# Kernel optimization log

Measured on AMD Instinct MI355X. Metric: run time of the kernel, lower is better.

Reference implementation:

```python
import jax, jax.numpy as jnp
import numpy as np

IN, H, OUT, T, B = 132, 1024, 132, 100, 256


def setup_inputs() -> dict:
    key = jax.random.key(0)
    ks = jax.random.split(key, 16)
    s_in = 1.0 / np.sqrt(H)
    def mk(k, shape):
        return jax.random.uniform(k, shape, jnp.float32, -s_in, s_in)
    inp = {
        "real_seq": jax.random.normal(ks[0], (B, T, IN), jnp.float32),
        "W_ih1": mk(ks[1], (4 * H, IN)), "W_hh1": mk(ks[2], (4 * H, H)),
        "b_ih1": mk(ks[3], (4 * H,)),   "b_hh1": mk(ks[4], (4 * H,)),
        "W_ih2": mk(ks[5], (4 * H, H)), "W_hh2": mk(ks[6], (4 * H, H)),
        "b_ih2": mk(ks[7], (4 * H,)),   "b_hh2": mk(ks[8], (4 * H,)),
        "W_ih3": mk(ks[9], (4 * H, H)), "W_hh3": mk(ks[10], (4 * H, H)),
        "b_ih3": mk(ks[11], (4 * H,)),  "b_hh3": mk(ks[12], (4 * H,)),
        "W_dec": mk(ks[13], (OUT, H)),  "b_dec": mk(ks[14], (OUT,)),
        "condition_num": 5, "groundtruth_num": 5,
    }
    return inp


def _lstm_cell(x, h, c, W_ih, W_hh, b_ih, b_hh):
    # torch LSTMCell: gates in (i, f, g, o) order
    gates = x @ W_ih.T + b_ih + h @ W_hh.T + b_hh
    i, f, g, o = jnp.split(gates, 4, axis=-1)
    i, f, o = jax.nn.sigmoid(i), jax.nn.sigmoid(f), jax.nn.sigmoid(o)
    g = jnp.tanh(g)
    c_new = f * c + i * g
    h_new = o * jnp.tanh(c_new)
    return h_new, c_new


def reference(real_seq, W_ih1, W_hh1, b_ih1, b_hh1,
              W_ih2, W_hh2, b_ih2, b_hh2,
              W_ih3, W_hh3, b_ih3, b_hh3,
              W_dec, b_dec, condition_num, groundtruth_num):
    batch, seq_len, _ = real_seq.shape
    # static teacher-forcing schedule: [1]*gt_num + [0]*cond_num, tiled
    gt = np.ones((100, groundtruth_num)); con = np.zeros((100, condition_num))
    cond = jnp.asarray(np.concatenate((gt, con), 1).reshape(-1)[:seq_len] == 1)

    z = jnp.zeros((batch, H), jnp.float32)
    init = (z, z, z, z, z, z, jnp.zeros((batch, OUT), jnp.float32))

    def step(carry, xs):
        h0, h1, h2, c0, c1, c2, prev_out = carry
        frame, use_gt = xs
        x = jnp.where(use_gt, frame, prev_out)
        # note: lstm2/lstm3 consume the OLD h0/h1, faithful to forward_lstm
        nh0, nc0 = _lstm_cell(x,  h0, c0, W_ih1, W_hh1, b_ih1, b_hh1)
        nh1, nc1 = _lstm_cell(h0, h1, c1, W_ih2, W_hh2, b_ih2, b_hh2)
        nh2, nc2 = _lstm_cell(h1, h2, c2, W_ih3, W_hh3, b_ih3, b_hh3)
        out = nh2 @ W_dec.T + b_dec
        return (nh0, nh1, nh2, nc0, nc1, nc2, out), out

    xs = (jnp.swapaxes(real_seq, 0, 1), cond)  # [T,B,IN], [T]
    _, outs = jax.lax.scan(step, init, xs)      # outs: [T,B,OUT]
    # torch concatenates along dim 1 each step -> [B, T*OUT]
    return jnp.swapaxes(outs, 0, 1).reshape(batch, seq_len * OUT)
```

## Files before the change

kernel.cpp:

```cpp
#include <hip/hip_runtime.h>
#include <math.h>

#define B_   256
#define T_   100
#define IN_  132
#define OUT_ 132
#define H_   1024
#define BH   ((size_t)B_ * H_)

typedef _Float16 f16;
typedef _Float16 f16x8 __attribute__((ext_vector_type(8)));
typedef float    f32x4 __attribute__((ext_vector_type(4)));

#define MFMA16(a, b, c) __builtin_amdgcn_mfma_f32_16x16x32_f16((a), (b), (c), 0, 0, 0)

#define AS1 __attribute__((address_space(1)))
#define AS3 __attribute__((address_space(3)))

__device__ __forceinline__ void gl_lds16(const void* g, void* l) {
    __builtin_amdgcn_global_load_lds((AS1 void*)g, (AS3 void*)l, 16, 0, 0);
}

__device__ __forceinline__ float sigmoidf_(float x) {
    return 1.0f / (1.0f + __expf(-x));
}
__device__ __forceinline__ float tanhf_(float x) {
    float e = __expf(2.0f * x);
    return 1.0f - 2.0f / (e + 1.0f);
}


__global__ void conv_pad(const float* __restrict__ src, f16* __restrict__ dst,
                         int src_rows, int src_k, int dst_k) {
    int k = blockIdx.x * 256 + threadIdx.x;
    int r = blockIdx.y;
    if (k >= dst_k) return;
    float v = (r < src_rows && k < src_k) ? src[(size_t)r * src_k + k] : 0.0f;
    dst[(size_t)r * dst_k + k] = (f16)v;
}

__global__ void convT_kernel(const float* __restrict__ Wd, f16* __restrict__ WdT) {
    int k = blockIdx.x * 256 + threadIdx.x;
    int m = blockIdx.y;
    if (k >= 160) return;
    float v = (k < IN_) ? Wd[(size_t)k * H_ + m] : 0.0f;
    WdT[(size_t)m * 160 + k] = (f16)v;
}

__global__ void bias_add_kernel(const float* __restrict__ a, const float* __restrict__ b,
                                float* __restrict__ dst, int n) {
    int i = blockIdx.x * 256 + threadIdx.x;
    if (i < n) dst[i] = a[i] + b[i];
}

__global__ void bfb_kernel(const float* __restrict__ Wih1, const float* __restrict__ bd,
                           float* __restrict__ bfb) {
    int j = blockIdx.x * 256 + threadIdx.x;
    if (j >= 4096) return;
    float s = 0.0f;
    for (int k = 0; k < IN_; ++k) s += Wih1[(size_t)j * IN_ + k] * bd[k];
    bfb[j] = s;
}

__global__ void zero_kernel(float* __restrict__ p, int n) {
    int i = blockIdx.x * blockDim.x + threadIdx.x;
    int st = gridDim.x * blockDim.x;
    for (; i < n; i += st) p[i] = 0.0f;
}

__global__ __launch_bounds__(256) void pack_w(const float* __restrict__ W,
                                              f16* __restrict__ Wpk, int wsel) {
    int jt = blockIdx.x, kk = blockIdx.y;
    f16* dst = Wpk + (((size_t)wsel * 64 + jt) * 32 + kk) * 2048;
    int u = threadIdx.x;
    int c = u >> 2, ch = u & 3;
    int row = ((c >> 4) & 3) * 1024 + jt * 16 + (c & 15);
    const float* s = W + (size_t)row * 1024 + kk * 32 + ch * 8;
    f16x8 v;
#pragma unroll
    for (int e = 0; e < 8; ++e) v[e] = (f16)s[e];
    *(f16x8*)(dst + (size_t)c * 32 + ch * 8) = v;
}

__global__ __launch_bounds__(256) void pack_wf16(const f16* __restrict__ W,
                                                 f16* __restrict__ Wpk, int wsel) {
    int jt = blockIdx.x, kk = blockIdx.y;
    f16* dst = Wpk + (((size_t)wsel * 64 + jt) * 32 + kk) * 2048;
    int u = threadIdx.x;
    int c = u >> 2, ch = u & 3;
    int row = ((c >> 4) & 3) * 1024 + jt * 16 + (c & 15);
    f16x8 v = *(const f16x8*)(W + (size_t)row * 1024 + kk * 32 + ch * 8);
    *(f16x8*)(dst + (size_t)c * 32 + ch * 8) = v;
}

__global__ __launch_bounds__(256) void pack_w0(const float* __restrict__ W,
                                               f16* __restrict__ W0pk) {
    int jt = blockIdx.x, kk = blockIdx.y;
    f16* dst = W0pk + ((size_t)jt * 5 + kk) * 2048;
    int u = threadIdx.x;
    int c = u >> 2, ch = u & 3;
    int row = ((c >> 4) & 3) * 1024 + jt * 16 + (c & 15);
    f16x8 v;
#pragma unroll
    for (int e = 0; e < 8; ++e) {
        int k = kk * 32 + ch * 8 + e;
        v[e] = (f16)((k < IN_) ? W[(size_t)row * IN_ + k] : 0.0f);
    }
    *(f16x8*)(dst + (size_t)c * 32 + ch * 8) = v;
}

__global__ __launch_bounds__(256) void pack_seq(const float* __restrict__ seq,
                                                f16* __restrict__ seqpk) {
    int kt = blockIdx.x, t = blockIdx.y;
    int b = threadIdx.x;
    f16* d = seqpk + (((size_t)t * 5 + kt) * 256 + b) * 32;
#pragma unroll
    for (int ch = 0; ch < 4; ++ch) {
        f16x8 v;
#pragma unroll
        for (int e = 0; e < 8; ++e) {
            int k = kt * 32 + ch * 8 + e;
            v[e] = (f16)((k < IN_) ? seq[((size_t)b * T_ + t) * IN_ + k] : 0.0f);
        }
        *(f16x8*)(d + ch * 8) = v;
    }
}

__global__ __launch_bounds__(256) void wfb_mfma(
    const f16* __restrict__ W0, const f16* __restrict__ WdT, f16* __restrict__ Wfb)
{
    const int m0 = blockIdx.x * 128;
    const int n0 = blockIdx.y * 128;
    const int tid  = threadIdx.x;
    const int lane = tid & 63;
    const int w    = tid >> 6;
    const int lx   = lane & 15;
    const int quad = lane >> 4;
    const int wrow = w >> 1, wcol = w & 1;

    __shared__ __align__(16) char lds[32768];

    auto stA = [&](int kt, int buf) {
        char* base = lds + buf * 16384;
#pragma unroll
        for (int i = 0; i < 2; ++i) {
            int r  = w * 32 + i * 16 + (lane >> 2);
            int sg = (lane & 3) ^ (r & 3);
            const f16* g = W0 + (size_t)(m0 + r) * 160 + kt * 32 + sg * 8;
            gl_lds16(g, base + (size_t)(w * 32 + i * 16) * 64);
        }
    };
    auto stB = [&](int kt, int buf) {
        char* base = lds + 8192 + buf * 16384;
#pragma unroll
        for (int i = 0; i < 2; ++i) {
            int r  = w * 32 + i * 16 + (lane >> 2);
            int sg = (lane & 3) ^ (r & 3);
            const f16* g = WdT + (size_t)(n0 + r) * 160 + kt * 32 + sg * 8;
            gl_lds16(g, base + (size_t)(w * 32 + i * 16) * 64);
        }
    };

    f32x4 acc[4][4];
#pragma unroll
    for (int m = 0; m < 4; ++m)
#pragma unroll
        for (int n = 0; n < 4; ++n) acc[m][n] = (f32x4){0.f, 0.f, 0.f, 0.f};

    stA(0, 0); stB(0, 0);
    for (int kt = 0; kt < 5; ++kt) {
        __syncthreads();
        if (kt + 1 < 5) { stA(kt + 1, (kt + 1) & 1); stB(kt + 1, (kt + 1) & 1); }
        const char* bA = lds + (kt & 1) * 16384;
        const char* bB = lds + 8192 + (kt & 1) * 16384;
        f16x8 af[4], bf[4];
#pragma unroll
        for (int m = 0; m < 4; ++m) {
            int R = wrow * 64 + m * 16 + lx;
            af[m] = *(const f16x8*)(bA + R * 64 + ((quad ^ (R & 3)) * 16));
        }
#pragma unroll
        for (int n = 0; n < 4; ++n) {
            int R = wcol * 64 + n * 16 + lx;
            bf[n] = *(const f16x8*)(bB + R * 64 + ((quad ^ (R & 3)) * 16));
        }
#pragma unroll
        for (int m = 0; m < 4; ++m)
#pragma unroll
            for (int n = 0; n < 4; ++n)
                acc[m][n] = MFMA16(af[m], bf[n], acc[m][n]);
    }

#pragma unroll
    for (int m = 0; m < 4; ++m)
#pragma unroll
        for (int n = 0; n < 4; ++n)
#pragma unroll
            for (int r = 0; r < 4; ++r) {
                int row = m0 + wrow * 64 + m * 16 + quad * 4 + r;
                int col = n0 + wcol * 64 + n * 16 + lx;
                Wfb[(size_t)row * H_ + col] = (f16)acc[m][n][r];
            }
}

__global__ __launch_bounds__(512) void step_mfma(
    const f16* __restrict__ seqpk,
    const f16* __restrict__ h2pkP,
    const f16* __restrict__ h01pkC,
    f16* __restrict__ h01pkN,
    f16* __restrict__ h2pkN,
    f16* __restrict__ histN,
    float* __restrict__ c_st,
    const f16* __restrict__ W0pk,
    const f16* __restrict__ Wpk,
    const float* __restrict__ bias_comb,
    const float* __restrict__ bfb,
    const int* __restrict__ cnum, const int* __restrict__ gnum,
    int t)
{
    extern __shared__ __align__(16) char lds[];

    const int jt   = blockIdx.x;
    const int l    = blockIdx.y;
    const int tid  = threadIdx.x;
    const int lane = tid & 63;
    const int w    = tid >> 6;
    const int team = w >> 2;
    const int mw   = w & 3;
    const int lx   = lane & 15;
    const int quad = lane >> 4;

    bool use_gt = false;
    int n0 = 32;
    const char *A0 = nullptr, *B0 = nullptr;
    const char* wbase = (const char*)Wpk + (size_t)jt * 131072;
    if (l == 0) {
        int cn = cnum[0], gn = gnum[0];
        use_gt = (t % (cn + gn)) < gn;
        if (use_gt)      { A0 = (const char*)(seqpk + (size_t)t * 40960);
                           B0 = (const char*)(W0pk + (size_t)jt * 10240); n0 = 5; }
        else if (t == 0) { n0 = 0; }
        else             { A0 = (const char*)h2pkP; B0 = wbase + (size_t)5 * 8388608; }
    } else if (l == 1) { A0 = (const char*)h01pkC;        B0 = wbase + (size_t)1 * 8388608; }
    else               { A0 = (const char*)(h01pkC + BH); B0 = wbase + (size_t)3 * 8388608; }
    const char* A1 = (l == 0) ? (const char*)h01pkC
                   : (l == 1) ? (const char*)(h01pkC + BH) : (const char*)h2pkP;
    const char* B1 = wbase + (size_t)((l == 0) ? 0 : (l == 1) ? 2 : 4) * 8388608;
    const int ntot = n0 + 32;
    const int nh   = (ntot + 1) >> 1;
    const int lo   = team ? nh : 0;
    const int hi   = team ? ntot : nh;
    const int n    = hi - lo;
    const int nmax = nh;

    char* tb = lds + team * 61440;

    auto stage = [&](int ktl, char* buf) {
        int itx = lo + ktl;
        int kk; const char *pa, *pb;
        if (itx < n0) { kk = itx;      pa = A0; pb = B0; }
        else          { kk = itx - n0; pa = A1; pb = B1; }
        pa += (size_t)kk * 16384;
        pb += (size_t)kk * 4096;
        const int s = lane & 3;
#pragma unroll
        for (int i = 0; i < 4; ++i) {
            int row16 = mw * 64 + i * 16;
            int r = row16 + (lane >> 2);
            gl_lds16(pa + r * 64 + ((s ^ (r & 3)) * 16), buf + row16 * 64);
        }
        {
            int c16 = mw * 16;
            int c = c16 + (lane >> 2);
            gl_lds16(pb + c * 64 + ((s ^ (c & 3)) * 16), buf + 16384 + c16 * 64);
        }
    };

    f32x4 acc[4][4];
#pragma unroll
    for (int m = 0; m < 4; ++m)
#pragma unroll
        for (int nn = 0; nn < 4; ++nn) acc[m][nn] = (f32x4){0.f, 0.f, 0.f, 0.f};

    if (n > 0) stage(0, tb);
    if (n > 1) stage(1, tb + 20480);

    auto ITER = [&](int kt, int p, int pn) {
        const bool act = kt < n;
        if (act) {
            if (kt < n - 1) asm volatile("s_waitcnt vmcnt(5)" ::: "memory");
            else            asm volatile("s_waitcnt vmcnt(0)" ::: "memory");
        }
        __builtin_amdgcn_s_barrier();

        f16x8 af[4], bf[4];
        if (act) {
            const char* bA = tb + p * 20480;
            const char* bB = bA + 16384;
#pragma unroll
            for (int m = 0; m < 4; ++m) {
                int R = mw * 64 + m * 16 + lx;
                af[m] = *(const f16x8*)(bA + R * 64 + ((quad ^ (R & 3)) * 16));
            }
#pragma unroll
            for (int nn = 0; nn < 4; ++nn) {
                int C = nn * 16 + lx;
                bf[nn] = *(const f16x8*)(bB + C * 64 + ((quad ^ (C & 3)) * 16));
            }
        }
        asm volatile("s_waitcnt lgkmcnt(0)" ::: "memory");
        __builtin_amdgcn_sched_barrier(0);

        if (act && kt + 2 < n) stage(kt + 2, tb + pn * 20480);

        if (act) {
            __builtin_amdgcn_s_setprio(1);
#pragma unroll
            for (int m = 0; m < 4; ++m)
#pragma unroll
                for (int nn = 0; nn < 4; ++nn)
                    acc[m][nn] = MFMA16(af[m], bf[nn], acc[m][nn]);
            __builtin_amdgcn_s_setprio(0);
        }
    };

    for (int kb = 0; kb < nmax; kb += 3) {
        ITER(kb, 0, 2);
        if (kb + 1 < nmax) ITER(kb + 1, 1, 0);
        if (kb + 2 < nmax) ITER(kb + 2, 2, 1);
    }

    __syncthreads();
    float* ex = (float*)lds;
    if (team == 1) {
#pragma unroll
        for (int m = 0; m < 4; ++m)
#pragma unroll
            for (int nn = 0; nn < 4; ++nn)
#pragma unroll
                for (int r = 0; r < 4; ++r) {
                    int row = mw * 64 + m * 16 + quad * 4 + r;
                    ex[(size_t)row * 64 + nn * 16 + lx] = acc[m][nn][r];
                }
    }
    __syncthreads();

    if (team == 0) {
        const int j = jt * 16 + lx;
        const float* bc = bias_comb + l * 4096;
        const bool addfb = (l == 0 && !use_gt && t > 0);
        float bi  = bc[j]        + (addfb ? bfb[j]        : 0.f);
        float bff = bc[1024 + j] + (addfb ? bfb[1024 + j] : 0.f);
        float bg  = bc[2048 + j] + (addfb ? bfb[2048 + j] : 0.f);
        float bo  = bc[3072 + j] + (addfb ? bfb[3072 + j] : 0.f);
#pragma unroll
        for (int m = 0; m < 4; ++m) {
#pragma unroll
            for (int r = 0; r < 4; ++r) {
                int b = mw * 64 + m * 16 + quad * 4 + r;
                const float* eb = ex + (size_t)b * 64;
                float gi = acc[m][0][r] + eb[lx]      + bi;
                float gf = acc[m][1][r] + eb[16 + lx] + bff;
                float gg = acc[m][2][r] + eb[32 + lx] + bg;
                float go = acc[m][3][r] + eb[48 + lx] + bo;
                size_t ix = ((size_t)l * B_ + b) * H_ + j;
                float cn2 = sigmoidf_(gf) * c_st[ix] + sigmoidf_(gi) * tanhf_(gg);
                c_st[ix] = cn2;
                float hv = sigmoidf_(go) * tanhf_(cn2);
                f16 hv16 = (f16)hv;
                size_t pix = ((size_t)(j >> 5) * 256 + b) * 32 + (j & 31);
                if (l == 2) { h2pkN[pix] = hv16; histN[(size_t)b * H_ + j] = hv16; }
                else        h01pkN[(size_t)l * BH + pix] = hv16;
            }
        }
    }
}

__global__ __launch_bounds__(256) void decode_mfma(
    const f16* __restrict__ hist,
    const f16* __restrict__ Wd16,
    const float* __restrict__ bd,
    float* __restrict__ dout)
{
    const int r0  = blockIdx.x * 128;
    const int nb0 = blockIdx.y * 32;
    const int tid  = threadIdx.x;
    const int lane = tid & 63;
    const int w    = tid >> 6;
    const int lx   = lane & 15;
    const int quad = lane >> 4;

    __shared__ __align__(16) char lds[20480];

    auto stA = [&](int kt, int buf) {
        char* base = lds + buf * 10240;
#pragma unroll
        for (int i = 0; i < 2; ++i) {
            int r  = w * 32 + i * 16 + (lane >> 2);
            int sg = (lane & 3) ^ (r & 3);
            const f16* g = hist + (size_t)(r0 + r) * H_ + kt * 32 + sg * 8;
            gl_lds16(g, base + (size_t)(w * 32 + i * 16) * 64);
        }
    };
    auto stB = [&](int kt, int buf) {
        char* base = lds + 8192 + buf * 10240;
        if (w < 2) {
            int r  = w * 16 + (lane >> 2);
            int sg = (lane & 3) ^ (r & 3);
            const f16* g = Wd16 + (size_t)(nb0 + r) * H_ + kt * 32 + sg * 8;
            gl_lds16(g, base + (size_t)(w * 16) * 64);
        }
    };

    f32x4 acc[2][2];
#pragma unroll
    for (int m = 0; m < 2; ++m)
#pragma unroll
        for (int n = 0; n < 2; ++n) acc[m][n] = (f32x4){0.f, 0.f, 0.f, 0.f};

    stA(0, 0); stB(0, 0);
    for (int kt = 0; kt < 32; ++kt) {
        __syncthreads();
        if (kt + 1 < 32) { stA(kt + 1, (kt + 1) & 1); stB(kt + 1, (kt + 1) & 1); }
        const char* bA = lds + (kt & 1) * 10240;
        const char* bB = lds + 8192 + (kt & 1) * 10240;
        f16x8 af[2], bf[2];
#pragma unroll
        for (int m = 0; m < 2; ++m) {
            int R = w * 32 + m * 16 + lx;
            af[m] = *(const f16x8*)(bA + R * 64 + ((quad ^ (R & 3)) * 16));
        }
#pragma unroll
        for (int n = 0; n < 2; ++n) {
            int R = n * 16 + lx;
            bf[n] = *(const f16x8*)(bB + R * 64 + ((quad ^ (R & 3)) * 16));
        }
#pragma unroll
        for (int m = 0; m < 2; ++m)
#pragma unroll
            for (int n = 0; n < 2; ++n)
                acc[m][n] = MFMA16(af[m], bf[n], acc[m][n]);
    }

#pragma unroll
    for (int n = 0; n < 2; ++n) {
        int nn = nb0 + n * 16 + lx;
        if (nn < OUT_) {
            float bv = bd[nn];
#pragma unroll
            for (int m = 0; m < 2; ++m)
#pragma unroll
                for (int r = 0; r < 4; ++r) {
                    int row = r0 + w * 32 + m * 16 + quad * 4 + r;
                    int tt = row >> 8, b = row & 255;
                    dout[(size_t)b * (T_ * OUT_) + (size_t)tt * OUT_ + nn] = acc[m][n][r] + bv;
                }
        }
    }
}


extern "C" void kernel_launch(void* const* d_in, const int* in_sizes, int n_in,
                              void* d_out, int out_size, void* d_ws, size_t ws_size,
                              hipStream_t stream) {
    const float* seq  = (const float*)d_in[0];
    const float* Wih1 = (const float*)d_in[1];
    const float* Whh1 = (const float*)d_in[2];
    const float* bih1 = (const float*)d_in[3];
    const float* bhh1 = (const float*)d_in[4];
    const float* Wih2 = (const float*)d_in[5];
    const float* Whh2 = (const float*)d_in[6];
    const float* bih2 = (const float*)d_in[7];
    const float* bhh2 = (const float*)d_in[8];
    const float* Wih3 = (const float*)d_in[9];
    const float* Whh3 = (const float*)d_in[10];
    const float* bih3 = (const float*)d_in[11];
    const float* bhh3 = (const float*)d_in[12];
    const float* Wd   = (const float*)d_in[13];
    const float* bd   = (const float*)d_in[14];
    const int*   cnum = (const int*)d_in[15];
    const int*   gnum = (const int*)d_in[16];

    char* p = (char*)d_ws;
    f16*  W0   = (f16*)p;  p += (size_t)4096 * 160 * 2;
    f16*  Wd16 = (f16*)p;  p += (size_t)160 * 1024 * 2;
    f16*  WdT  = (f16*)p;  p += (size_t)1024 * 160 * 2;
    f16*  Wfb  = (f16*)p;  p += (size_t)4096 * 1024 * 2;
    float* bias_comb = (float*)p; p += (size_t)3 * 4096 * 4;
    float* bfb = (float*)p; p += (size_t)4096 * 4;
    f16*  hist = (f16*)p;  p += (size_t)100 * BH * 2;
    f16*  h01pkA = (f16*)p; p += (size_t)2 * BH * 2;
    f16*  h2pkA  = (f16*)p; p += (size_t)BH * 2;
    float* c_st  = (float*)p; p += (size_t)3 * BH * 4;
    f16*  h01pkB = (f16*)p; p += (size_t)2 * BH * 2;
    f16*  h2pkB  = (f16*)p; p += (size_t)BH * 2;
    f16*  Wpk   = (f16*)p; p += (size_t)6 * 64 * 32 * 2048 * 2;
    f16*  W0pk  = (f16*)p; p += (size_t)64 * 5 * 2048 * 2;
    f16*  seqpk = (f16*)p; p += (size_t)T_ * 5 * 256 * 32 * 2;

    const int zero_floats = (int)(((size_t)3 * BH * 2 + (size_t)3 * BH * 4) / 4);

    hipFuncSetAttribute((const void*)step_mfma,
                        hipFuncAttributeMaxDynamicSharedMemorySize, 122880);

    conv_pad<<<dim3(1, 4096), 256, 0, stream>>>(Wih1, W0, 4096, IN_, 160);
    conv_pad<<<dim3(4, 160), 256, 0, stream>>>(Wd, Wd16, OUT_, H_, H_);
    convT_kernel<<<dim3(1, 1024), 256, 0, stream>>>(Wd, WdT);
    bias_add_kernel<<<16, 256, 0, stream>>>(bih1, bhh1, bias_comb + 0 * 4096, 4096);
    bias_add_kernel<<<16, 256, 0, stream>>>(bih2, bhh2, bias_comb + 1 * 4096, 4096);
    bias_add_kernel<<<16, 256, 0, stream>>>(bih3, bhh3, bias_comb + 2 * 4096, 4096);
    bfb_kernel<<<16, 256, 0, stream>>>(Wih1, bd, bfb);
    wfb_mfma<<<dim3(32, 8), 256, 0, stream>>>(W0, WdT, Wfb);
    pack_w<<<dim3(64, 32), 256, 0, stream>>>(Whh1, Wpk, 0);
    pack_w<<<dim3(64, 32), 256, 0, stream>>>(Wih2, Wpk, 1);
    pack_w<<<dim3(64, 32), 256, 0, stream>>>(Whh2, Wpk, 2);
    pack_w<<<dim3(64, 32), 256, 0, stream>>>(Wih3, Wpk, 3);
    pack_w<<<dim3(64, 32), 256, 0, stream>>>(Whh3, Wpk, 4);
    pack_wf16<<<dim3(64, 32), 256, 0, stream>>>(Wfb, Wpk, 5);
    pack_w0<<<dim3(64, 5), 256, 0, stream>>>(Wih1, W0pk);
    pack_seq<<<dim3(5, T_), 256, 0, stream>>>(seq, seqpk);
    zero_kernel<<<512, 256, 0, stream>>>((float*)h01pkA, zero_floats);

    f16 *h01C = h01pkA, *h01N = h01pkB, *h2P = h2pkA, *h2N = h2pkB;
    for (int t = 0; t < T_; ++t) {
        step_mfma<<<dim3(64, 3), 512, 122880, stream>>>(
            seqpk, h2P, h01C, h01N, h2N, hist + (size_t)t * BH, c_st,
            W0pk, Wpk, bias_comb, bfb, cnum, gnum, t);
        f16* tmp;
        tmp = h01C; h01C = h01N; h01N = tmp;
        tmp = h2P;  h2P  = h2N;  h2N  = tmp;
    }

    decode_mfma<<<dim3(200, 5), 256, 0, stream>>>(hist, Wd16, bd, (float*)d_out);
}
```

Measured before the change: 3.332 ms.

## Fuse per-timestep LSTM launches into one persistent kernel with grid barrier

Replaces 100 separate step kernel launches with a single persistent kernel of 192 blocks that loops over timesteps and synchronises the whole grid through an atomic counter barrier. The cell state moves from a global array into per-thread registers, which removes its global read and write each step, and the bias loads are hoisted out of the time loop. This removes launch gaps and per-launch setup. In exchange, all 192 blocks must be co-resident (one block per CU, with the large LDS footprint) or the barrier deadlocks, and the spin barrier adds atomic traffic.

New measurement: 9.631 ms. 189% more time.

```diff
diff --git a/kernel.cpp b/kernel.cpp
--- a/kernel.cpp
+++ b/kernel.cpp
@@ -7,6 +7,7 @@
 #define OUT_ 132
 #define H_   1024
 #define BH   ((size_t)B_ * H_)
+#define NBLK 192u
 
 typedef _Float16 f16;
 typedef _Float16 f16x8 __attribute__((ext_vector_type(8)));
@@ -203,20 +204,19 @@
             }
 }
 
-__global__ __launch_bounds__(512) void step_mfma(
+__global__ __launch_bounds__(512) void step_persist(
     const f16* __restrict__ seqpk,
-    const f16* __restrict__ h2pkP,
-    const f16* __restrict__ h01pkC,
-    f16* __restrict__ h01pkN,
-    f16* __restrict__ h2pkN,
-    f16* __restrict__ histN,
-    float* __restrict__ c_st,
+    f16* __restrict__ h01pkA,
+    f16* __restrict__ h01pkB,
+    f16* __restrict__ h2pkA,
+    f16* __restrict__ h2pkB,
+    f16* __restrict__ hist,
     const f16* __restrict__ W0pk,
     const f16* __restrict__ Wpk,
     const float* __restrict__ bias_comb,
     const float* __restrict__ bfb,
     const int* __restrict__ cnum, const int* __restrict__ gnum,
-    int t)
+    unsigned* __restrict__ bar)
 {
     extern __shared__ __align__(16) char lds[];
 
@@ -230,149 +230,189 @@
     const int lx   = lane & 15;
     const int quad = lane >> 4;
 
-    bool use_gt = false;
-    int n0 = 32;
-    const char *A0 = nullptr, *B0 = nullptr;
+    const int cn = cnum[0], gn = gnum[0];
     const char* wbase = (const char*)Wpk + (size_t)jt * 131072;
-    if (l == 0) {
-        int cn = cnum[0], gn = gnum[0];
-        use_gt = (t % (cn + gn)) < gn;
-        if (use_gt)      { A0 = (const char*)(seqpk + (size_t)t * 40960);
-                           B0 = (const char*)(W0pk + (size_t)jt * 10240); n0 = 5; }
-        else if (t == 0) { n0 = 0; }
-        else             { A0 = (const char*)h2pkP; B0 = wbase + (size_t)5 * 8388608; }
-    } else if (l == 1) { A0 = (const char*)h01pkC;        B0 = wbase + (size_t)1 * 8388608; }
-    else               { A0 = (const char*)(h01pkC + BH); B0 = wbase + (size_t)3 * 8388608; }
-    const char* A1 = (l == 0) ? (const char*)h01pkC
-                   : (l == 1) ? (const char*)(h01pkC + BH) : (const char*)h2pkP;
-    const char* B1 = wbase + (size_t)((l == 0) ? 0 : (l == 1) ? 2 : 4) * 8388608;
-    const int ntot = n0 + 32;
-    const int nh   = (ntot + 1) >> 1;
-    const int lo   = team ? nh : 0;
-    const int hi   = team ? ntot : nh;
-    const int n    = hi - lo;
-    const int nmax = nh;
+    const char* Bfb   = wbase + (size_t)5 * 8388608;
+    const char* B0nt  = (l == 0) ? Bfb
+                      : (l == 1) ? (wbase + (size_t)1 * 8388608)
+                                 : (wbase + (size_t)3 * 8388608);
+    const char* B1w   = wbase + (size_t)((l == 0) ? 0 : (l == 1) ? 2 : 4) * 8388608;
+    const char* B0tf  = (const char*)(W0pk + (size_t)jt * 10240);
 
     char* tb = lds + team * 61440;
-
-    auto stage = [&](int ktl, char* buf) {
-        int itx = lo + ktl;
-        int kk; const char *pa, *pb;
-        if (itx < n0) { kk = itx;      pa = A0; pb = B0; }
-        else          { kk = itx - n0; pa = A1; pb = B1; }
-        pa += (size_t)kk * 16384;
-        pb += (size_t)kk * 4096;
-        const int s = lane & 3;
-#pragma unroll
-        for (int i = 0; i < 4; ++i) {
-            int row16 = mw * 64 + i * 16;
-            int r = row16 + (lane >> 2);
-            gl_lds16(pa + r * 64 + ((s ^ (r & 3)) * 16), buf + row16 * 64);
-        }
-        {
-            int c16 = mw * 16;
-            int c = c16 + (lane >> 2);
-            gl_lds16(pb + c * 64 + ((s ^ (c & 3)) * 16), buf + 16384 + c16 * 64);
-        }
-    };
-
-    f32x4 acc[4][4];
+    float* ex = (float*)lds;
+
+    const int j = jt * 16 + lx;
+    const float* bc = bias_comb + l * 4096;
+    const float bi0  = bc[j],        fbi  = bfb[j];
+    const float bff0 = bc[1024 + j], fbf  = bfb[1024 + j];
+    const float bg0  = bc[2048 + j], fbg  = bfb[2048 + j];
+    const float bo0  = bc[3072 + j], fbo  = bfb[3072 + j];
+
+    float creg[4][4];
 #pragma unroll
     for (int m = 0; m < 4; ++m)
 #pragma unroll
-        for (int nn = 0; nn < 4; ++nn) acc[m][nn] = (f32x4){0.f, 0.f, 0.f, 0.f};
-
-    if (n > 0) stage(0, tb);
-    if (n > 1) stage(1, tb + 20480);
-
-    auto ITER = [&](int kt, int p, int pn) {
-        const bool act = kt < n;
-        if (act) {
-            if (kt < n - 1) asm volatile("s_waitcnt vmcnt(5)" ::: "memory");
-            else            asm volatile("s_waitcnt vmcnt(0)" ::: "memory");
-        }
-        __builtin_amdgcn_s_barrier();
-
-        f16x8 af[4], bf[4];
-        if (act) {
-            const char* bA = tb + p * 20480;
-            const char* bB = bA + 16384;
+        for (int r = 0; r < 4; ++r) creg[m][r] = 0.f;
+
+    f16 *h01C = h01pkA, *h01N = h01pkB, *h2P = h2pkA, *h2N = h2pkB;
+
+    for (int t = 0; t < T_; ++t) {
+        bool use_gt = false;
+        int n0 = 32;
+        const char *A0 = nullptr, *B0 = nullptr;
+        if (l == 0) {
+            use_gt = (t % (cn + gn)) < gn;
+            if (use_gt)      { A0 = (const char*)(seqpk + (size_t)t * 40960);
+                               B0 = B0tf; n0 = 5; }
+            else if (t == 0) { n0 = 0; }
+            else             { A0 = (const char*)h2P; B0 = B0nt; }
+        } else if (l == 1) { A0 = (const char*)h01C;        B0 = B0nt; }
+        else               { A0 = (const char*)(h01C + BH); B0 = B0nt; }
+        const char* A1 = (l == 0) ? (const char*)h01C
+                       : (l == 1) ? (const char*)(h01C + BH) : (const char*)h2P;
+        const int ntot = n0 + 32;
+        const int nh   = (ntot + 1) >> 1;
+        const int lo   = team ? nh : 0;
+        const int hi   = team ? ntot : nh;
+        const int n    = hi - lo;
+        const int nmax = nh;
+
+        auto stage = [&](int ktl, char* buf) {
+            int itx = lo + ktl;
+            int kk; const char *pa, *pb;
+            if (itx < n0) { kk = itx;      pa = A0; pb = B0; }
+            else          { kk = itx - n0; pa = A1; pb = B1w; }
+            pa += (size_t)kk * 16384;
+            pb += (size_t)kk * 4096;
+            const int s = lane & 3;
+#pragma unroll
+            for (int i = 0; i < 4; ++i) {
+                int row16 = mw * 64 + i * 16;
+                int r = row16 + (lane >> 2);
+                gl_lds16(pa + r * 64 + ((s ^ (r & 3)) * 16), buf + row16 * 64);
+            }
+            {
+                int c16 = mw * 16;
+                int c = c16 + (lane >> 2);
+                gl_lds16(pb + c * 64 + ((s ^ (c & 3)) * 16), buf + 16384 + c16 * 64);
+            }
+        };
+
+        f32x4 acc[4][4];
+#pragma unroll
+        for (int m = 0; m < 4; ++m)
+#pragma unroll
+            for (int nn = 0; nn < 4; ++nn) acc[m][nn] = (f32x4){0.f, 0.f, 0.f, 0.f};
+
+        if (n > 0) stage(0, tb);
+        if (n > 1) stage(1, tb + 20480);
+
+        auto ITER = [&](int kt, int p, int pn) {
+            const bool act = kt < n;
+            if (act) {
+                if (kt < n - 1) asm volatile("s_waitcnt vmcnt(5)" ::: "memory");
+                else            asm volatile("s_waitcnt vmcnt(0)" ::: "memory");
+            }
+            __builtin_amdgcn_s_barrier();
+
+            f16x8 af[4], bf[4];
+            if (act) {
+                const char* bA = tb + p * 20480;
+                const char* bB = bA + 16384;
+#pragma unroll
+                for (int m = 0; m < 4; ++m) {
+                    int R = mw * 64 + m * 16 + lx;
+                    af[m] = *(const f16x8*)(bA + R * 64 + ((quad ^ (R & 3)) * 16));
+                }
+#pragma unroll
+                for (int nn = 0; nn < 4; ++nn) {
+                    int C = nn * 16 + lx;
+                    bf[nn] = *(const f16x8*)(bB + C * 64 + ((quad ^ (C & 3)) * 16));
+                }
+            }
+            asm volatile("s_waitcnt lgkmcnt(0)" ::: "memory");
+            __builtin_amdgcn_sched_barrier(0);
+
+            if (act && kt + 2 < n) stage(kt + 2, tb + pn * 20480);
+
+            if (act) {
+                __builtin_amdgcn_s_setprio(1);
+#pragma unroll
+                for (int m = 0; m < 4; ++m)
+#pragma unroll
+                    for (int nn = 0; nn < 4; ++nn)
+                        acc[m][nn] = MFMA16(af[m], bf[nn], acc[m][nn]);
+                __builtin_amdgcn_s_setprio(0);
+            }
+        };
+
+        for (int kb = 0; kb < nmax; kb += 3) {
+            ITER(kb, 0, 2);
+            if (kb + 1 < nmax) ITER(kb + 1, 1, 0);
+            if (kb + 2 < nmax) ITER(kb + 2, 2, 1);
+        }
+
+        __syncthreads();
+        if (team == 1) {
+#pragma unroll
+            for (int m = 0; m < 4; ++m)
+#pragma unroll
+                for (int nn = 0; nn < 4; ++nn)
+#pragma unroll
+                    for (int r = 0; r < 4; ++r) {
+                        int row = mw * 64 + m * 16 + quad * 4 + r;
+                        ex[(size_t)row * 64 + nn * 16 + lx] = acc[m][nn][r];
+                    }
+        }
+        __syncthreads();
+
+        if (team == 0) {
+            const bool addfb = (l == 0 && !use_gt && t > 0);
+            float bi  = bi0  + (addfb ? fbi : 0.f);
+            float bff = bff0 + (addfb ? fbf : 0.f);
+            float bg  = bg0  + (addfb ? fbg : 0.f);
+            float bo  = bo0  + (addfb ? fbo : 0.f);
+            f16* histN = hist + (size_t)t * BH;
 #pragma unroll
             for (int m = 0; m < 4; ++m) {
-                int R = mw * 64 + m * 16 + lx;
-                af[m] = *(const f16x8*)(bA + R * 64 + ((quad ^ (R & 3)) * 16));
-            }
-#pragma unroll
-            for (int nn = 0; nn < 4; ++nn) {
-                int C = nn * 16 + lx;
-                bf[nn] = *(const f16x8*)(bB + C * 64 + ((quad ^ (C & 3)) * 16));
-            }
-        }
-        asm volatile("s_waitcnt lgkmcnt(0)" ::: "memory");
-        __builtin_amdgcn_sched_barrier(0);
-
-        if (act && kt + 2 < n) stage(kt + 2, tb + pn * 20480);
-
-        if (act) {
-            __builtin_amdgcn_s_setprio(1);
-#pragma unroll
-            for (int m = 0; m < 4; ++m)
-#pragma unroll
-                for (int nn = 0; nn < 4; ++nn)
-                    acc[m][nn] = MFMA16(af[m], bf[nn], acc[m][nn]);
-            __builtin_amdgcn_s_setprio(0);
-        }
-    };
-
-    for (int kb = 0; kb < nmax; kb += 3) {
-        ITER(kb, 0, 2);
-        if (kb + 1 < nmax) ITER(kb + 1, 1, 0);
-        if (kb + 2 < nmax) ITER(kb + 2, 2, 1);
-    }
-
-    __syncthreads();
-    float* ex = (float*)lds;
-    if (team == 1) {
-#pragma unroll
-        for (int m = 0; m < 4; ++m)
-#pragma unroll
-            for (int nn = 0; nn < 4; ++nn)
 #pragma unroll
                 for (int r = 0; r < 4; ++r) {
-                    int row = mw * 64 + m * 16 + quad * 4 + r;
-                    ex[(size_t)row * 64 + nn * 16 + lx] = acc[m][nn][r];
+                    int b = mw * 64 + m * 16 + quad * 4 + r;
+                    const float* eb = ex + (size_t)b * 64;
+                    float gi = acc[m][0][r] + eb[lx]      + bi;
+                    float gf = acc[m][1][r] + eb[16 + lx] + bff;
+                    float gg = acc[m][2][r] + eb[32 + lx] + bg;
+                    float go = acc[m][3][r] + eb[48 + lx] + bo;
+                    float cn2 = sigmoidf_(gf) * creg[m][r] + sigmoidf_(gi) * tanhf_(gg);
+                    creg[m][r] = cn2;
+                    float hv = sigmoidf_(go) * tanhf_(cn2);
+                    f16 hv16 = (f16)hv;
+                    size_t pix = ((size_t)(j >> 5) * 256 + b) * 32 + (j & 31);
+                    if (l == 2) { h2N[pix] = hv16; histN[(size_t)b * H_ + j] = hv16; }
+                    else        h01N[(size_t)l * BH + pix] = hv16;
                 }
-    }
-    __syncthreads();
-
-    if (team == 0) {
-        const int j = jt * 16 + lx;
-        const float* bc = bias_comb + l * 4096;
-        const bool addfb = (l == 0 && !use_gt && t > 0);
-        float bi  = bc[j]        + (addfb ? bfb[j]        : 0.f);
-        float bff = bc[1024 + j] + (addfb ? bfb[1024 + j] : 0.f);
-        float bg  = bc[2048 + j] + (addfb ? bfb[2048 + j] : 0.f);
-        float bo  = bc[3072 + j] + (addfb ? bfb[3072 + j] : 0.f);
-#pragma unroll
-        for (int m = 0; m < 4; ++m) {
-#pragma unroll
-            for (int r = 0; r < 4; ++r) {
-                int b = mw * 64 + m * 16 + quad * 4 + r;
-                const float* eb = ex + (size_t)b * 64;
-                float gi = acc[m][0][r] + eb[lx]      + bi;
-                float gf = acc[m][1][r] + eb[16 + lx] + bff;
-                float gg = acc[m][2][r] + eb[32 + lx] + bg;
-                float go = acc[m][3][r] + eb[48 + lx] + bo;
-                size_t ix = ((size_t)l * B_ + b) * H_ + j;
-                float cn2 = sigmoidf_(gf) * c_st[ix] + sigmoidf_(gi) * tanhf_(gg);
-                c_st[ix] = cn2;
-                float hv = sigmoidf_(go) * tanhf_(cn2);
-                f16 hv16 = (f16)hv;
-                size_t pix = ((size_t)(j >> 5) * 256 + b) * 32 + (j & 31);
-                if (l == 2) { h2pkN[pix] = hv16; histN[(size_t)b * H_ + j] = hv16; }
-                else        h01pkN[(size_t)l * BH + pix] = hv16;
-            }
-        }
+            }
+        }
+
+        if (t + 1 < T_) {
+            __threadfence();
+            __syncthreads();
+            if (tid == 0) {
+                __hip_atomic_fetch_add(bar, 1u, __ATOMIC_ACQ_REL,
+                                       __HIP_MEMORY_SCOPE_AGENT);
+                unsigned target = NBLK * (unsigned)(t + 1);
+                while (__hip_atomic_load(bar, __ATOMIC_ACQUIRE,
+                                         __HIP_MEMORY_SCOPE_AGENT) < target)
+                    __builtin_amdgcn_s_sleep(2);
+            }
+            __syncthreads();
+            __threadfence();
+        }
+
+        f16* tmp;
+        tmp = h01C; h01C = h01N; h01N = tmp;
+        tmp = h2P;  h2P  = h2N;  h2N  = tmp;
     }
 }
 
@@ -491,16 +531,16 @@
     f16*  hist = (f16*)p;  p += (size_t)100 * BH * 2;
     f16*  h01pkA = (f16*)p; p += (size_t)2 * BH * 2;
     f16*  h2pkA  = (f16*)p; p += (size_t)BH * 2;
-    float* c_st  = (float*)p; p += (size_t)3 * BH * 4;
+    unsigned* bar = (unsigned*)p; p += 256;
     f16*  h01pkB = (f16*)p; p += (size_t)2 * BH * 2;
     f16*  h2pkB  = (f16*)p; p += (size_t)BH * 2;
     f16*  Wpk   = (f16*)p; p += (size_t)6 * 64 * 32 * 2048 * 2;
     f16*  W0pk  = (f16*)p; p += (size_t)64 * 5 * 2048 * 2;
     f16*  seqpk = (f16*)p; p += (size_t)T_ * 5 * 256 * 32 * 2;
 
-    const int zero_floats = (int)(((size_t)3 * BH * 2 + (size_t)3 * BH * 4) / 4);
-
-    hipFuncSetAttribute((const void*)step_mfma,
+    const int zero_floats = (int)(((size_t)3 * BH * 2 + 256) / 4);
+
+    hipFuncSetAttribute((const void*)step_persist,
                         hipFuncAttributeMaxDynamicSharedMemorySize, 122880);
 
     conv_pad<<<dim3(1, 4096), 256, 0, stream>>>(Wih1, W0, 4096, IN_, 160);
@@ -521,15 +561,9 @@
     pack_seq<<<dim3(5, T_), 256, 0, stream>>>(seq, seqpk);
     zero_kernel<<<512, 256, 0, stream>>>((float*)h01pkA, zero_floats);
 
-    f16 *h01C = h01pkA, *h01N = h01pkB, *h2P = h2pkA, *h2N = h2pkB;
-    for (int t = 0; t < T_; ++t) {
-        step_mfma<<<dim3(64, 3), 512, 122880, stream>>>(
-            seqpk, h2P, h01C, h01N, h2N, hist + (size_t)t * BH, c_st,
-            W0pk, Wpk, bias_comb, bfb, cnum, gnum, t);
-        f16* tmp;
-        tmp = h01C; h01C = h01N; h01N = tmp;
-        tmp = h2P;  h2P  = h2N;  h2N  = tmp;
-    }
+    step_persist<<<dim3(64, 3), 512, 122880, stream>>>(
+        seqpk, h01pkA, h01pkB, h2pkA, h2pkB, hist,
+        W0pk, Wpk, bias_comb, bfb, cnum, gnum, bar);
 
     decode_mfma<<<dim3(200, 5), 256, 0, stream>>>(hist, Wd16, bd, (float*)d_out);
 }
```
